# Kernel optimization log

Measured on AMD Instinct MI355X. Metric: run time of the kernel, lower is better.

The kernel has to match this reference:

```python
import jax, jax.numpy as jnp
import numpy as np

DT = 0.1  # Euler timestep (init kwarg)

def setup_inputs() -> dict:
    key = jax.random.key(0)
    ks = jax.random.split(key, 6)
    B, L, S, U, H = 1024, 512, 64, 32, 512
    return {
        "initial_state": jax.random.normal(ks[0], (B, S), dtype=jnp.float32),
        "control_inputs": jax.random.normal(ks[1], (B, L, U), dtype=jnp.float32),
        "W1": jax.random.normal(ks[2], (S + U, H), dtype=jnp.float32) * (1.0 / np.sqrt(S + U)),
        "b1": jnp.zeros((H,), dtype=jnp.float32),
        "W2": jax.random.normal(ks[3], (H, S), dtype=jnp.float32) * (1.0 / np.sqrt(H)),
        "b2": jnp.zeros((S,), dtype=jnp.float32),
    }

def reference(initial_state, control_inputs, W1, b1, W2, b2):
    # Euler integration: state_{t+1} = state_t + dt * f(state_t, u_t)
    # f is a 2-layer tanh MLP on the concatenated [state, control].
    def step(state, u):
        z = jnp.concatenate([state, u], axis=-1)        # (B, S+U)
        diff = jnp.tanh(z @ W1 + b1) @ W2 + b2          # (B, S)
        new_state = state + diff * DT
        return new_state, new_state

    u_seq = jnp.swapaxes(control_inputs, 0, 1)          # (L, B, U)
    _, states = jax.lax.scan(step, initial_state, u_seq)  # (L, B, S)
    return jnp.swapaxes(states, 0, 1)                   # (B, L, S)
```

## Files before the change

### kernel.cpp

```cpp
#include <hip/hip_runtime.h>
#include <hip/hip_fp16.h>


typedef _Float16 f16;
typedef __attribute__((ext_vector_type(4))) _Float16 f16x4;
typedef __attribute__((ext_vector_type(8))) _Float16 f16x8;
typedef __attribute__((ext_vector_type(4))) float f32x4;

#define MFMA16(a, b, c) __builtin_amdgcn_mfma_f32_16x16x32_f16((a), (b), (c), 0, 0, 0)

__device__ __forceinline__ float tanh_fast(float x) {
    float t = __builtin_amdgcn_exp2f(x * 2.885390081777927f);
    float r = __builtin_amdgcn_rcpf(t + 1.0f);
    return __builtin_fmaf(-2.0f, r, 1.0f);
}

__global__ __launch_bounds__(512, 2)
void euler_kernel(const float* __restrict__ init,
                  const float* __restrict__ uin,
                  const float* __restrict__ W1,
                  const float* __restrict__ b1,
                  const float* __restrict__ W2,
                  const float* __restrict__ b2,
                  float* __restrict__ out) {
    const int L = 512, S = 64, U = 32, H = 512;
    const int tid  = threadIdx.x;
    const int lane = tid & 63;
    const int w    = tid >> 6;
    const int g    = lane >> 4;
    const int r16  = lane & 15;
    const int b0   = blockIdx.x * 16;

    __shared__ f16 zbuf[16][200];
    __shared__ f16 hbuf[16][520];

    f16x8 W1F[6][4];
    #pragma unroll
    for (int kk = 0; kk < 6; ++kk)
      #pragma unroll
      for (int nf = 0; nf < 4; ++nf)
        #pragma unroll
        for (int j = 0; j < 8; ++j) {
            int k  = kk * 32 + g * 8 + j;
            int kr = (k < 128) ? (k & 63) : (64 + (k & 31));
            W1F[kk][nf][j] = (f16)W1[kr * H + w * 64 + nf * 16 + r16];
        }
    f32x4 b1v[4];
    #pragma unroll
    for (int nf = 0; nf < 4; ++nf)
        b1v[nf] = *(const f32x4*)&b1[w * 64 + nf * 16 + g * 4];

    f16x8 W2F[16];
    f32x4 b2v = (f32x4){0.f, 0.f, 0.f, 0.f};
    f32x4 stateF = (f32x4){0.f, 0.f, 0.f, 0.f};
    f32x4 ua0 = (f32x4){0.f, 0.f, 0.f, 0.f}, ua1 = ua0;
    if (w < 4) {
        #pragma unroll
        for (int kk = 0; kk < 16; ++kk)
          #pragma unroll
          for (int j = 0; j < 8; ++j) {
              int k = kk * 32 + g * 8 + j;
              W2F[kk][j] = (f16)W2[k * S + w * 16 + r16];
          }
        b2v = *(const f32x4*)&b2[w * 16 + g * 4];
        stateF = *(const f32x4*)&init[(size_t)(b0 + r16) * S + w * 16 + g * 4];
        f16x4 sh, sl;
        #pragma unroll
        for (int j = 0; j < 4; ++j) {
            sh[j] = (f16)stateF[j];
            sl[j] = (f16)(stateF[j] - (float)sh[j]);
        }
        *(f16x4*)&zbuf[r16][w * 16 + g * 4]      = sh;
        *(f16x4*)&zbuf[r16][64 + w * 16 + g * 4] = sl;
    } else {
        const float* up = uin + (size_t)(b0 + r16) * L * U + g * 8;
        f32x4 u0 = *(const f32x4*)up;
        f32x4 u1 = *(const f32x4*)(up + 4);
        f16x8 uh, ul;
        #pragma unroll
        for (int j = 0; j < 4; ++j) {
            f16 h0 = (f16)u0[j]; uh[j] = h0;     ul[j] = (f16)(u0[j] - (float)h0);
            f16 h1 = (f16)u1[j]; uh[4 + j] = h1; ul[4 + j] = (f16)(u1[j] - (float)h1);
        }
        *(f16x8*)&zbuf[r16][128 + g * 8] = uh;
        *(f16x8*)&zbuf[r16][160 + g * 8] = ul;
        ua0 = *(const f32x4*)(up + U);
        ua1 = *(const f32x4*)(up + U + 4);
    }
    __syncthreads();

    #pragma unroll 1
    for (int t = 0; t < L; ++t) {
        f16x8 zf[6];
        #pragma unroll
        for (int kk = 0; kk < 6; ++kk)
            zf[kk] = *(const f16x8*)&zbuf[r16][kk * 32 + g * 8];
        f32x4 acc1[4];
        #pragma unroll
        for (int nf = 0; nf < 4; ++nf) acc1[nf] = b1v[nf];
        #pragma unroll
        for (int kk = 0; kk < 6; ++kk)
          #pragma unroll
          for (int nf = 0; nf < 4; ++nf)
            acc1[nf] = MFMA16(W1F[kk][nf], zf[kk], acc1[nf]);
        #pragma unroll
        for (int nf = 0; nf < 4; ++nf) {
            f16x4 hv;
            #pragma unroll
            for (int j = 0; j < 4; ++j) hv[j] = (f16)tanh_fast(acc1[nf][j]);
            *(f16x4*)&hbuf[r16][w * 64 + nf * 16 + g * 4] = hv;
        }
        __syncthreads();

        if (w < 4) {
            f32x4 accA = (f32x4){0.f, 0.f, 0.f, 0.f};
            f32x4 accB = (f32x4){0.f, 0.f, 0.f, 0.f};
            #pragma unroll
            for (int kk = 0; kk < 8; ++kk) {
                f16x8 hf = *(const f16x8*)&hbuf[r16][kk * 32 + g * 8];
                accA = MFMA16(W2F[kk], hf, accA);
            }
            #pragma unroll
            for (int kk = 8; kk < 16; ++kk) {
                f16x8 hf = *(const f16x8*)&hbuf[r16][kk * 32 + g * 8];
                accB = MFMA16(W2F[kk], hf, accB);
            }
            f16x4 sh, sl;
            #pragma unroll
            for (int j = 0; j < 4; ++j) {
                float d = (accA[j] + accB[j]) + b2v[j];
                float s = __builtin_fmaf(0.1f, d, stateF[j]);
                stateF[j] = s;
                sh[j] = (f16)s;
                sl[j] = (f16)(s - (float)sh[j]);
            }
            *(f32x4*)&out[((size_t)(b0 + r16) * L + t) * S + w * 16 + g * 4] = stateF;
            *(f16x4*)&zbuf[r16][w * 16 + g * 4]      = sh;
            *(f16x4*)&zbuf[r16][64 + w * 16 + g * 4] = sl;
        } else {
            if (t + 1 < L) {
                f16x8 uh, ul;
                #pragma unroll
                for (int j = 0; j < 4; ++j) {
                    f16 h0 = (f16)ua0[j]; uh[j] = h0;     ul[j] = (f16)(ua0[j] - (float)h0);
                    f16 h1 = (f16)ua1[j]; uh[4 + j] = h1; ul[4 + j] = (f16)(ua1[j] - (float)h1);
                }
                *(f16x8*)&zbuf[r16][128 + g * 8] = uh;
                *(f16x8*)&zbuf[r16][160 + g * 8] = ul;
            }
            if (t + 2 < L) {
                const float* up = uin + (size_t)(b0 + r16) * L * U + (size_t)(t + 2) * U + g * 8;
                ua0 = *(const f32x4*)up;
                ua1 = *(const f32x4*)(up + 4);
            }
        }
        __syncthreads();
    }
}

extern "C" void kernel_launch(void* const* d_in, const int* in_sizes, int n_in,
                              void* d_out, int out_size, void* d_ws, size_t ws_size,
                              hipStream_t stream) {
    const float* init = (const float*)d_in[0];
    const float* uin  = (const float*)d_in[1];
    const float* W1   = (const float*)d_in[2];
    const float* b1   = (const float*)d_in[3];
    const float* W2   = (const float*)d_in[4];
    const float* b2   = (const float*)d_in[5];
    euler_kernel<<<dim3(64), dim3(512), 0, stream>>>(init, uin, W1, b1, W2, b2,
                                                     (float*)d_out);
}
```

Before: 664.7 us.

## Split second-layer GEMM across all waves with register-resident hidden activations

Each wave now computes a partial second-layer product straight from its own tanh outputs kept in registers. It permutes the W1 columns so the first GEMM's accumulator layout matches the operand layout the second MFMA expects. Partial sums from the 8 waves go through shared memory in fp32 and are reduced by 4 waves, replacing the hidden-activation round trip and the 16-MFMA serial chain on only 4 waves. The z buffer is also laid out in MFMA-fragment order for conflict-free vector loads. The cost is an 8-way LDS reduction per step, a larger fp32 partial buffer, and fewer waves doing the control-input conversion.

After: 600.6 us. 9.7% less time.

```diff
diff --git a/kernel.cpp b/kernel.cpp
--- a/kernel.cpp
+++ b/kernel.cpp
@@ -31,38 +31,46 @@
     const int r16  = lane & 15;
     const int b0   = blockIdx.x * 16;
 
-    __shared__ f16 zbuf[16][200];
-    __shared__ f16 hbuf[16][520];
+    __shared__ f16   zbuf[6 * 64 * 8];
+    __shared__ float pbuf[8 * 16 * 16 * 4];
 
     f16x8 W1F[6][4];
     #pragma unroll
     for (int kk = 0; kk < 6; ++kk)
       #pragma unroll
-      for (int nf = 0; nf < 4; ++nf)
-        #pragma unroll
-        for (int j = 0; j < 8; ++j) {
-            int k  = kk * 32 + g * 8 + j;
-            int kr = (k < 128) ? (k & 63) : (64 + (k & 31));
-            W1F[kk][nf][j] = (f16)W1[kr * H + w * 64 + nf * 16 + r16];
-        }
+      for (int nf = 0; nf < 4; ++nf) {
+          const int hcol = w * 64 + 32 * (nf >> 1) + 8 * (r16 >> 2) + 4 * (nf & 1) + (r16 & 3);
+          #pragma unroll
+          for (int j = 0; j < 8; ++j) {
+              int k  = kk * 32 + g * 8 + j;
+              int kr = (k < 128) ? (k & 63) : (64 + (k & 31));
+              W1F[kk][nf][j] = (f16)W1[kr * H + hcol];
+          }
+      }
     f32x4 b1v[4];
     #pragma unroll
     for (int nf = 0; nf < 4; ++nf)
-        b1v[nf] = *(const f32x4*)&b1[w * 64 + nf * 16 + g * 4];
+        b1v[nf] = *(const f32x4*)&b1[w * 64 + 32 * (nf >> 1) + 4 * (nf & 1) + 8 * g];
 
-    f16x8 W2F[16];
+    f16x8 W2F[2][4];
+    #pragma unroll
+    for (int a = 0; a < 2; ++a)
+      #pragma unroll
+      for (int nf2 = 0; nf2 < 4; ++nf2)
+        #pragma unroll
+        for (int j = 0; j < 8; ++j) {
+            int k = w * 64 + a * 32 + g * 8 + j;
+            W2F[a][nf2][j] = (f16)W2[k * S + nf2 * 16 + r16];
+        }
+
     f32x4 b2v = (f32x4){0.f, 0.f, 0.f, 0.f};
     f32x4 stateF = (f32x4){0.f, 0.f, 0.f, 0.f};
     f32x4 ua0 = (f32x4){0.f, 0.f, 0.f, 0.f}, ua1 = ua0;
+    const int schunk = (w >> 1) * 64 + ((w & 1) * 2 + (g >> 1)) * 16 + r16;
+    const int soff   = (g & 1) * 4;
+
     if (w < 4) {
-        #pragma unroll
-        for (int kk = 0; kk < 16; ++kk)
-          #pragma unroll
-          for (int j = 0; j < 8; ++j) {
-              int k = kk * 32 + g * 8 + j;
-              W2F[kk][j] = (f16)W2[k * S + w * 16 + r16];
-          }
-        b2v = *(const f32x4*)&b2[w * 16 + g * 4];
+        b2v    = *(const f32x4*)&b2[w * 16 + g * 4];
         stateF = *(const f32x4*)&init[(size_t)(b0 + r16) * S + w * 16 + g * 4];
         f16x4 sh, sl;
         #pragma unroll
@@ -70,20 +78,25 @@
             sh[j] = (f16)stateF[j];
             sl[j] = (f16)(stateF[j] - (float)sh[j]);
         }
-        *(f16x4*)&zbuf[r16][w * 16 + g * 4]      = sh;
-        *(f16x4*)&zbuf[r16][64 + w * 16 + g * 4] = sl;
-    } else {
+        *(f16x4*)&zbuf[schunk * 8 + soff]         = sh;
+        *(f16x4*)&zbuf[(schunk + 128) * 8 + soff] = sl;
+    } else if (w == 4 || w == 5) {
         const float* up = uin + (size_t)(b0 + r16) * L * U + g * 8;
         f32x4 u0 = *(const f32x4*)up;
         f32x4 u1 = *(const f32x4*)(up + 4);
-        f16x8 uh, ul;
-        #pragma unroll
-        for (int j = 0; j < 4; ++j) {
-            f16 h0 = (f16)u0[j]; uh[j] = h0;     ul[j] = (f16)(u0[j] - (float)h0);
-            f16 h1 = (f16)u1[j]; uh[4 + j] = h1; ul[4 + j] = (f16)(u1[j] - (float)h1);
+        f16x8 uv;
+        if (w == 4) {
+            #pragma unroll
+            for (int j = 0; j < 4; ++j) { uv[j] = (f16)u0[j]; uv[4 + j] = (f16)u1[j]; }
+            *(f16x8*)&zbuf[(256 + lane) * 8] = uv;
+        } else {
+            #pragma unroll
+            for (int j = 0; j < 4; ++j) {
+                uv[j]     = (f16)(u0[j] - (float)(f16)u0[j]);
+                uv[4 + j] = (f16)(u1[j] - (float)(f16)u1[j]);
+            }
+            *(f16x8*)&zbuf[(320 + lane) * 8] = uv;
         }
-        *(f16x8*)&zbuf[r16][128 + g * 8] = uh;
-        *(f16x8*)&zbuf[r16][160 + g * 8] = ul;
         ua0 = *(const f32x4*)(up + U);
         ua1 = *(const f32x4*)(up + U + 4);
     }
@@ -94,7 +107,7 @@
         f16x8 zf[6];
         #pragma unroll
         for (int kk = 0; kk < 6; ++kk)
-            zf[kk] = *(const f16x8*)&zbuf[r16][kk * 32 + g * 8];
+            zf[kk] = *(const f16x8*)&zbuf[(kk * 64 + lane) * 8];
         f32x4 acc1[4];
         #pragma unroll
         for (int nf = 0; nf < 4; ++nf) acc1[nf] = b1v[nf];
@@ -103,50 +116,60 @@
           #pragma unroll
           for (int nf = 0; nf < 4; ++nf)
             acc1[nf] = MFMA16(W1F[kk][nf], zf[kk], acc1[nf]);
+        f16x8 hb[2];
         #pragma unroll
-        for (int nf = 0; nf < 4; ++nf) {
-            f16x4 hv;
-            #pragma unroll
-            for (int j = 0; j < 4; ++j) hv[j] = (f16)tanh_fast(acc1[nf][j]);
-            *(f16x4*)&hbuf[r16][w * 64 + nf * 16 + g * 4] = hv;
-        }
+        for (int a = 0; a < 2; ++a)
+          #pragma unroll
+          for (int j8 = 0; j8 < 8; ++j8)
+            hb[a][j8] = (f16)tanh_fast(acc1[a * 2 + (j8 >> 2)][j8 & 3]);
+        f32x4 acc2[4];
+        #pragma unroll
+        for (int nf2 = 0; nf2 < 4; ++nf2) acc2[nf2] = (f32x4){0.f, 0.f, 0.f, 0.f};
+        #pragma unroll
+        for (int a = 0; a < 2; ++a)
+          #pragma unroll
+          for (int nf2 = 0; nf2 < 4; ++nf2)
+            acc2[nf2] = MFMA16(W2F[a][nf2], hb[a], acc2[nf2]);
+        #pragma unroll
+        for (int nf2 = 0; nf2 < 4; ++nf2)
+            *(f32x4*)&pbuf[(w * 256 + nf2 * 64 + lane) * 4] = acc2[nf2];
         __syncthreads();
 
         if (w < 4) {
-            f32x4 accA = (f32x4){0.f, 0.f, 0.f, 0.f};
-            f32x4 accB = (f32x4){0.f, 0.f, 0.f, 0.f};
+            f32x4 sum = *(const f32x4*)&pbuf[(w * 64 + lane) * 4];
             #pragma unroll
-            for (int kk = 0; kk < 8; ++kk) {
-                f16x8 hf = *(const f16x8*)&hbuf[r16][kk * 32 + g * 8];
-                accA = MFMA16(W2F[kk], hf, accA);
-            }
-            #pragma unroll
-            for (int kk = 8; kk < 16; ++kk) {
-                f16x8 hf = *(const f16x8*)&hbuf[r16][kk * 32 + g * 8];
-                accB = MFMA16(W2F[kk], hf, accB);
+            for (int ww = 1; ww < 8; ++ww) {
+                f32x4 p = *(const f32x4*)&pbuf[(ww * 256 + w * 64 + lane) * 4];
+                #pragma unroll
+                for (int j = 0; j < 4; ++j) sum[j] += p[j];
             }
             f16x4 sh, sl;
             #pragma unroll
             for (int j = 0; j < 4; ++j) {
-                float d = (accA[j] + accB[j]) + b2v[j];
+                float d = sum[j] + b2v[j];
                 float s = __builtin_fmaf(0.1f, d, stateF[j]);
                 stateF[j] = s;
                 sh[j] = (f16)s;
                 sl[j] = (f16)(s - (float)sh[j]);
             }
             *(f32x4*)&out[((size_t)(b0 + r16) * L + t) * S + w * 16 + g * 4] = stateF;
-            *(f16x4*)&zbuf[r16][w * 16 + g * 4]      = sh;
-            *(f16x4*)&zbuf[r16][64 + w * 16 + g * 4] = sl;
-        } else {
+            *(f16x4*)&zbuf[schunk * 8 + soff]         = sh;
+            *(f16x4*)&zbuf[(schunk + 128) * 8 + soff] = sl;
+        } else if (w == 4 || w == 5) {
             if (t + 1 < L) {
-                f16x8 uh, ul;
-                #pragma unroll
-                for (int j = 0; j < 4; ++j) {
-                    f16 h0 = (f16)ua0[j]; uh[j] = h0;     ul[j] = (f16)(ua0[j] - (float)h0);
-                    f16 h1 = (f16)ua1[j]; uh[4 + j] = h1; ul[4 + j] = (f16)(ua1[j] - (float)h1);
+                f16x8 uv;
+                if (w == 4) {
+                    #pragma unroll
+                    for (int j = 0; j < 4; ++j) { uv[j] = (f16)ua0[j]; uv[4 + j] = (f16)ua1[j]; }
+                    *(f16x8*)&zbuf[(256 + lane) * 8] = uv;
+                } else {
+                    #pragma unroll
+                    for (int j = 0; j < 4; ++j) {
+                        uv[j]     = (f16)(ua0[j] - (float)(f16)ua0[j]);
+                        uv[4 + j] = (f16)(ua1[j] - (float)(f16)ua1[j]);
+                    }
+                    *(f16x8*)&zbuf[(320 + lane) * 8] = uv;
                 }
-                *(f16x8*)&zbuf[r16][128 + g * 8] = uh;
-                *(f16x8*)&zbuf[r16][160 + g * 8] = ul;
             }
             if (t + 2 < L) {
                 const float* up = uin + (size_t)(b0 + r16) * L * U + (size_t)(t + 2) * U + g * 8;
```
